# Performance work log

Measured on AMD Instinct MI355X. Metric: run time of the kernel, lower is better.

## Reference

```python
import jax, jax.numpy as jnp
import numpy as np

ALPHA = 0.2  # LeakyReLU negative slope (init arg `alpha`)
N, F_IN, F_OUT = 8192, 512, 256


def setup_inputs() -> dict:
    key = jax.random.key(0)
    k1, k2, k3, k4 = jax.random.split(key, 4)
    x = jax.random.normal(k1, (N, F_IN), dtype=jnp.float32)
    adj = jax.random.randint(k2, (N, N), 0, 2, dtype=jnp.int32)
    W = jax.random.normal(k3, (F_IN, F_OUT), dtype=jnp.float32) * (1.0 / np.sqrt(F_IN))
    a = jax.random.normal(k4, (2 * F_OUT, 1), dtype=jnp.float32) * (1.0 / np.sqrt(F_IN))
    return {"x": x, "adj": adj, "W": W, "a": a}


def reference(x, adj, W, a):
    h = x @ W  # [N, F_OUT]
    f_out = W.shape[1]
    # e[i,j] = LeakyReLU(a1 . h_i + a2 . h_j); computed without the O(N^2*2F) concat
    f1 = h @ a[:f_out, 0]   # [N]
    f2 = h @ a[f_out:, 0]   # [N]
    s = f1[:, None] + f2[None, :]  # [N, N]
    e = jnp.where(s >= 0, s, ALPHA * s)
    # Faithful to the source bug: -9e15 * zeros_like == zeros, so masked entries are 0.0
    att = jnp.where(adj > 0, e, jnp.zeros((), dtype=e.dtype))
    att = jax.nn.softmax(att, axis=1)
    # dropout is identity in eval mode
    h_prime = att @ h  # [N, F_OUT]
    return jax.nn.elu(h_prime)  # concat=True branch
```

## Files before the change

### kernel.cpp

```cpp
#include <hip/hip_runtime.h>
#include <stdint.h>

#define NN 8192
#define FIN 512
#define FOUT 256
#define ALPHA 0.2f
#define KSPLIT 4

typedef float f32x4 __attribute__((ext_vector_type(4)));
typedef short s16x8 __attribute__((ext_vector_type(8)));

__device__ __forceinline__ uint16_t f2bf(float f) {
  union { float f; uint32_t u; } v; v.f = f;
  uint32_t u = v.u + 0x7fffu + ((v.u >> 16) & 1u);
  return (uint16_t)(u >> 16);
}

__global__ __launch_bounds__(256) void k_wa(const float* __restrict__ W,
                                            const float* __restrict__ a,
                                            float* __restrict__ wa1, float* __restrict__ wa2) {
  __shared__ float a1[256], a2[256];
  int tid = threadIdx.x;
  a1[tid] = a[tid];
  a2[tid] = a[tid + 256];
  __syncthreads();
  int m = blockIdx.x * 256 + tid;
  const float* wrow = W + (size_t)m * FOUT;
  float s1 = 0.f, s2 = 0.f;
  for (int k = 0; k < FOUT; k += 4) {
    f32x4 v = *(const f32x4*)(wrow + k);
#pragma unroll
    for (int i = 0; i < 4; i++) {
      s1 += v[i] * a1[k + i];
      s2 += v[i] * a2[k + i];
    }
  }
  wa1[m] = s1; wa2[m] = s2;
}

__global__ __launch_bounds__(256) void k_f1f2(const float* __restrict__ x,
                                              const float* __restrict__ wa1,
                                              const float* __restrict__ wa2,
                                              float* __restrict__ f1, float* __restrict__ f2,
                                              float* __restrict__ e1p, float* __restrict__ e1n,
                                              float* __restrict__ e2p, float* __restrict__ e2n,
                                              uint16_t* __restrict__ xb,
                                              float* __restrict__ l_arr) {
  __shared__ float s1[512], s2[512];
  int tid = threadIdx.x;
  if (tid < 4) l_arr[blockIdx.x * 4 + tid] = 0.f;
  s1[tid] = wa1[tid]; s1[tid + 256] = wa1[tid + 256];
  s2[tid] = wa2[tid]; s2[tid + 256] = wa2[tid + 256];
  __syncthreads();
  int w = tid >> 6, l = tid & 63;
  int row = blockIdx.x * 4 + w;
  const float* xr = x + (size_t)row * FIN + l * 8;
  f32x4 v0 = *(const f32x4*)xr;
  f32x4 v1 = *(const f32x4*)(xr + 4);
  uint4 pk;
  pk.x = (uint32_t)f2bf(v0[0]) | ((uint32_t)f2bf(v0[1]) << 16);
  pk.y = (uint32_t)f2bf(v0[2]) | ((uint32_t)f2bf(v0[3]) << 16);
  pk.z = (uint32_t)f2bf(v1[0]) | ((uint32_t)f2bf(v1[1]) << 16);
  pk.w = (uint32_t)f2bf(v1[2]) | ((uint32_t)f2bf(v1[3]) << 16);
  *(uint4*)(xb + (size_t)row * FIN + l * 8) = pk;
  int kb = l * 8;
  float d1 = 0.f, d2 = 0.f;
#pragma unroll
  for (int i = 0; i < 4; i++) {
    d1 += v0[i] * s1[kb + i] + v1[i] * s1[kb + 4 + i];
    d2 += v0[i] * s2[kb + i] + v1[i] * s2[kb + 4 + i];
  }
#pragma unroll
  for (int off = 32; off; off >>= 1) {
    d1 += __shfl_down(d1, off);
    d2 += __shfl_down(d2, off);
  }
  if (l == 0) {
    f1[row] = d1; f2[row] = d2;
    e1p[row] = __expf(d1);
    e1n[row] = __expf(ALPHA * d1);
    e2p[row] = __expf(d2);
    e2n[row] = __expf(ALPHA * d2);
  }
}

__global__ __launch_bounds__(256) void k_prep_wt(const float* __restrict__ W,
                                                 uint16_t* __restrict__ wt) {
  int idx = blockIdx.x * 256 + threadIdx.x;
  int f  = idx >> 7;
  int k4 = (idx & 127) * 4;
  ushort4 o;
  o.x = f2bf(W[(size_t)(k4 + 0) * FOUT + f]);
  o.y = f2bf(W[(size_t)(k4 + 1) * FOUT + f]);
  o.z = f2bf(W[(size_t)(k4 + 2) * FOUT + f]);
  o.w = f2bf(W[(size_t)(k4 + 3) * FOUT + f]);
  *(ushort4*)(wt + (size_t)f * FIN + k4) = o;
}

__global__ __launch_bounds__(256, 2) void k_gemm_h(const uint16_t* __restrict__ xb,
                                                   const uint16_t* __restrict__ wt,
                                                   uint16_t* __restrict__ h) {
  __shared__ uint16_t Xs[64][40];
  __shared__ uint16_t Ws[128][40];
  int i0 = blockIdx.x * 64;
  int f0 = blockIdx.y * 128;
  int tid = threadIdx.x;
  int w = tid >> 6, l = tid & 63;
  int wr = w >> 1, wc = w & 1;
  int q = l >> 4, r16 = l & 15;
  f32x4 acc[2][4];
#pragma unroll
  for (int a = 0; a < 2; a++)
#pragma unroll
    for (int b = 0; b < 4; b++) acc[a][b] = (f32x4)0.f;

  int srow = tid >> 2, sch = tid & 3;
  for (int k0 = 0; k0 < FIN; k0 += 32) {
    uint4 xv = *(const uint4*)(xb + (size_t)(i0 + srow) * FIN + k0 + sch * 8);
    *(uint4*)(&Xs[srow][sch * 8]) = xv;
#pragma unroll
    for (int r = 0; r < 2; r++) {
      int idx = tid + r * 256;
      int rr = idx >> 2, cc = idx & 3;
      uint4 vw = *(const uint4*)(wt + (size_t)(f0 + rr) * FIN + k0 + cc * 8);
      *(uint4*)(&Ws[rr][cc * 8]) = vw;
    }
    __syncthreads();
    s16x8 A[2], B[4];
#pragma unroll
    for (int a = 0; a < 2; a++) A[a] = *(const s16x8*)(&Xs[wr * 32 + a * 16 + r16][q * 8]);
#pragma unroll
    for (int b = 0; b < 4; b++) B[b] = *(const s16x8*)(&Ws[wc * 64 + b * 16 + r16][q * 8]);
#pragma unroll
    for (int a = 0; a < 2; a++)
#pragma unroll
      for (int b = 0; b < 4; b++)
        acc[a][b] = __builtin_amdgcn_mfma_f32_16x16x32_bf16(A[a], B[b], acc[a][b], 0, 0, 0);
    __syncthreads();
  }
#pragma unroll
  for (int a = 0; a < 2; a++)
#pragma unroll
    for (int b = 0; b < 4; b++)
#pragma unroll
      for (int reg = 0; reg < 4; reg++) {
        int row = i0 + wr * 32 + a * 16 + q * 4 + reg;
        int col = f0 + wc * 64 + b * 16 + r16;
        h[(size_t)row * FOUT + col] = f2bf(acc[a][b][reg]);
      }
}

__global__ __launch_bounds__(256) void k_transpose(const uint16_t* __restrict__ h,
                                                   uint16_t* __restrict__ ht) {
  __shared__ uint16_t T[64][72];
  int i0 = blockIdx.x * 64, f0 = blockIdx.y * 64;
  int tid = threadIdx.x;
#pragma unroll
  for (int p = 0; p < 2; p++) {
    int idx = tid + p * 256;
    int r = idx >> 3, c8 = idx & 7;
    uint4 v = *(const uint4*)(h + (size_t)(i0 + r) * FOUT + f0 + c8 * 8);
    *(uint4*)(&T[r][c8 * 8]) = v;
  }
  __syncthreads();
#pragma unroll
  for (int p = 0; p < 2; p++) {
    int idx = tid + p * 256;
    int fr = idx >> 3, ic8 = idx & 7;
    s16x8 v;
#pragma unroll
    for (int j = 0; j < 8; j++) v[j] = (short)T[ic8 * 8 + j][fr];
    *(s16x8*)(ht + (size_t)(f0 + fr) * NN + i0 + ic8 * 8) = v;
  }
}

__global__ __launch_bounds__(256, 2) void k_att(const int* __restrict__ adj,
                                                const uint16_t* __restrict__ ht,
                                                const float* __restrict__ f1,
                                                const float* __restrict__ f2,
                                                const float* __restrict__ e1p,
                                                const float* __restrict__ e1n,
                                                const float* __restrict__ e2p,
                                                const float* __restrict__ e2n,
                                                float* __restrict__ l_arr,
                                                float* __restrict__ part) {
  __shared__ uint16_t Ps[64][72];
  __shared__ uint16_t Hs[256][72];
  int i0 = blockIdx.x * 64;
  int jbase = blockIdx.y * (NN / KSPLIT);
  int tid = threadIdx.x;
  int w = tid >> 6, l = tid & 63;
  int q = l >> 4, r16 = l & 15;
  int prow = tid >> 2, pch = tid & 3;
  int srow = tid >> 3, sch = tid & 7;
  float negf1 = -f1[i0 + prow];
  float e1pi = e1p[i0 + prow];
  float e1ni = e1n[i0 + prow];
  float lsum = 0.f;
  f32x4 acc[4][4];
#pragma unroll
  for (int a = 0; a < 4; a++)
#pragma unroll
    for (int b = 0; b < 4; b++) acc[a][b] = (f32x4)0.f;

  for (int s = 0; s < NN / KSPLIT; s += 64) {
    int j0 = jbase + s;
    uint4 hv[8];
#pragma unroll
    for (int p = 0; p < 8; p++)
      hv[p] = *(const uint4*)(ht + (size_t)(p * 32 + srow) * NN + j0 + sch * 8);
    const int* ap = adj + (size_t)(i0 + prow) * NN + j0 + pch * 16;
    int4 A0 = *(const int4*)ap;
    int4 A1 = *(const int4*)(ap + 4);
    int4 A2 = *(const int4*)(ap + 8);
    int4 A3 = *(const int4*)(ap + 12);
    const float* fp = f2 + j0 + pch * 16;
    f32x4 F0 = *(const f32x4*)fp;
    f32x4 F1 = *(const f32x4*)(fp + 4);
    f32x4 F2 = *(const f32x4*)(fp + 8);
    f32x4 F3 = *(const f32x4*)(fp + 12);
    const float* gp = e2p + j0 + pch * 16;
    f32x4 P0 = *(const f32x4*)gp;
    f32x4 P1 = *(const f32x4*)(gp + 4);
    f32x4 P2 = *(const f32x4*)(gp + 8);
    f32x4 P3 = *(const f32x4*)(gp + 12);
    const float* gn = e2n + j0 + pch * 16;
    f32x4 Q0 = *(const f32x4*)gn;
    f32x4 Q1 = *(const f32x4*)(gn + 4);
    f32x4 Q2 = *(const f32x4*)(gn + 8);
    f32x4 Q3 = *(const f32x4*)(gn + 12);
    s16x8 pv0, pv1;
#define PC(dst, kk, Ac, Fc, Pc, Nc) { bool c_ = (Fc) >= negf1; \
      float p_ = ((Ac) != 0) ? (c_ ? e1pi : e1ni) * (c_ ? (Pc) : (Nc)) : 1.0f; \
      lsum += p_; dst[kk] = (short)f2bf(p_); }
    PC(pv0, 0, A0.x, F0[0], P0[0], Q0[0]); PC(pv0, 1, A0.y, F0[1], P0[1], Q0[1]);
    PC(pv0, 2, A0.z, F0[2], P0[2], Q0[2]); PC(pv0, 3, A0.w, F0[3], P0[3], Q0[3]);
    PC(pv0, 4, A1.x, F1[0], P1[0], Q1[0]); PC(pv0, 5, A1.y, F1[1], P1[1], Q1[1]);
    PC(pv0, 6, A1.z, F1[2], P1[2], Q1[2]); PC(pv0, 7, A1.w, F1[3], P1[3], Q1[3]);
    PC(pv1, 0, A2.x, F2[0], P2[0], Q2[0]); PC(pv1, 1, A2.y, F2[1], P2[1], Q2[1]);
    PC(pv1, 2, A2.z, F2[2], P2[2], Q2[2]); PC(pv1, 3, A2.w, F2[3], P2[3], Q2[3]);
    PC(pv1, 4, A3.x, F3[0], P3[0], Q3[0]); PC(pv1, 5, A3.y, F3[1], P3[1], Q3[1]);
    PC(pv1, 6, A3.z, F3[2], P3[2], Q3[2]); PC(pv1, 7, A3.w, F3[3], P3[3], Q3[3]);
#undef PC
    *(s16x8*)(&Ps[prow][pch * 16]) = pv0;
    *(s16x8*)(&Ps[prow][pch * 16 + 8]) = pv1;
#pragma unroll
    for (int p = 0; p < 8; p++)
      *(uint4*)(&Hs[p * 32 + srow][sch * 8]) = hv[p];
    __syncthreads();
#pragma unroll
    for (int c = 0; c < 2; c++) {
      s16x8 Af[4], Bf[4];
#pragma unroll
      for (int a = 0; a < 4; a++) Af[a] = *(const s16x8*)(&Ps[a * 16 + r16][c * 32 + q * 8]);
#pragma unroll
      for (int b = 0; b < 4; b++) Bf[b] = *(const s16x8*)(&Hs[w * 64 + b * 16 + r16][c * 32 + q * 8]);
#pragma unroll
      for (int a = 0; a < 4; a++)
#pragma unroll
        for (int b = 0; b < 4; b++)
          acc[a][b] = __builtin_amdgcn_mfma_f32_16x16x32_bf16(Af[a], Bf[b], acc[a][b], 0, 0, 0);
    }
    __syncthreads();
  }

  lsum += __shfl_down(lsum, 2);
  lsum += __shfl_down(lsum, 1);
  if (pch == 0) atomicAdd(&l_arr[i0 + prow], lsum);

  float* pb = part + (size_t)blockIdx.y * ((size_t)NN * FOUT);
#pragma unroll
  for (int a = 0; a < 4; a++)
#pragma unroll
    for (int b = 0; b < 4; b++)
#pragma unroll
      for (int reg = 0; reg < 4; reg++) {
        int row = i0 + a * 16 + q * 4 + reg;
        int col = w * 64 + b * 16 + r16;
        pb[(size_t)row * FOUT + col] = acc[a][b][reg];
      }
}

__global__ __launch_bounds__(256) void k_combine(const float* __restrict__ part,
                                                 const float* __restrict__ l_arr,
                                                 float* __restrict__ out) {
  int idx = (blockIdx.x * 256 + threadIdx.x) * 4;
  float r = 1.0f / l_arr[idx >> 8];
  f32x4 v0 = *(const f32x4*)(part + 0 * (size_t)(NN * FOUT) + idx);
  f32x4 v1 = *(const f32x4*)(part + 1 * (size_t)(NN * FOUT) + idx);
  f32x4 v2 = *(const f32x4*)(part + 2 * (size_t)(NN * FOUT) + idx);
  f32x4 v3 = *(const f32x4*)(part + 3 * (size_t)(NN * FOUT) + idx);
  f32x4 o;
#pragma unroll
  for (int i = 0; i < 4; i++) {
    float v = (v0[i] + v1[i] + v2[i] + v3[i]) * r;
    o[i] = v > 0.f ? v : (__expf(v) - 1.f);
  }
  *(f32x4*)(out + idx) = o;
}

extern "C" void kernel_launch(void* const* d_in, const int* in_sizes, int n_in,
                              void* d_out, int out_size, void* d_ws, size_t ws_size,
                              hipStream_t stream) {
  const float* x   = (const float*)d_in[0];
  const int*   adj = (const int*)d_in[1];
  const float* W   = (const float*)d_in[2];
  const float* a   = (const float*)d_in[3];
  float* out = (float*)d_out;

  char* ws = (char*)d_ws;
  float*    wa1   = (float*)ws;
  float*    wa2   = wa1 + 512;
  float*    f1    = wa2 + 512;
  float*    f2    = f1 + NN;
  float*    l_arr = f2 + NN;
  float*    e1p   = l_arr + NN;
  float*    e1n   = e1p + NN;
  float*    e2p   = e1n + NN;
  float*    e2n   = e2p + NN;
  uint16_t* wt    = (uint16_t*)(e2n + NN);
  uint16_t* xb    = wt + (size_t)FOUT * FIN;
  uint16_t* h     = xb + (size_t)NN * FIN;
  uint16_t* ht    = h + (size_t)NN * FOUT;
  float*    part  = (float*)(ht + (size_t)NN * FOUT);

  k_wa<<<2, 256, 0, stream>>>(W, a, wa1, wa2);
  k_f1f2<<<NN / 4, 256, 0, stream>>>(x, wa1, wa2, f1, f2, e1p, e1n, e2p, e2n, xb, l_arr);
  k_prep_wt<<<128, 256, 0, stream>>>(W, wt);
  k_gemm_h<<<dim3(NN / 64, 2), 256, 0, stream>>>(xb, wt, h);
  k_transpose<<<dim3(NN / 64, FOUT / 64), 256, 0, stream>>>(h, ht);
  k_att<<<dim3(NN / 64, KSPLIT), 256, 0, stream>>>(adj, ht, f1, f2, e1p, e1n, e2p, e2n, l_arr, part);
  k_combine<<<NN * FOUT / 1024, 256, 0, stream>>>(part, l_arr, out);
}
```

Measured before the change: 522.7 us.

## Restructure attention kernel with adjacency prefetch, double-buffered P, direct H fragment loads

The attention kernel now prefetches the next adjacency tile into registers while computing the current one, and double-buffers the probability tile in shared memory. It drops the shared-memory staging of H and reads B fragments straight from global memory. The j-split doubles to 8 and occupancy is raised to 3 blocks per CU, to expose more parallelism and cut synchronisation. The e2 exponentials are packed as two bf16 values in one word to halve those loads, at some precision cost. The H GEMM tile shrinks to 64x64 for more blocks, and the combine kernel reads twice as many partial buffers.

```diff
diff --git a/kernel.cpp b/kernel.cpp
--- a/kernel.cpp
+++ b/kernel.cpp
@@ -5,10 +5,13 @@
 #define FIN 512
 #define FOUT 256
 #define ALPHA 0.2f
-#define KSPLIT 4
+#define KSPLIT 8
+#define JT 64
+#define NT ((NN / KSPLIT) / JT)
 
 typedef float f32x4 __attribute__((ext_vector_type(4)));
 typedef short s16x8 __attribute__((ext_vector_type(8)));
+typedef uint32_t u32x4 __attribute__((ext_vector_type(4)));
 
 __device__ __forceinline__ uint16_t f2bf(float f) {
   union { float f; uint32_t u; } v; v.f = f;
@@ -43,7 +46,7 @@
                                               const float* __restrict__ wa2,
                                               float* __restrict__ f1, float* __restrict__ f2,
                                               float* __restrict__ e1p, float* __restrict__ e1n,
-                                              float* __restrict__ e2p, float* __restrict__ e2n,
+                                              uint32_t* __restrict__ epack,
                                               uint16_t* __restrict__ xb,
                                               float* __restrict__ l_arr) {
   __shared__ float s1[512], s2[512];
@@ -79,8 +82,7 @@
     f1[row] = d1; f2[row] = d2;
     e1p[row] = __expf(d1);
     e1n[row] = __expf(ALPHA * d1);
-    e2p[row] = __expf(d2);
-    e2n[row] = __expf(ALPHA * d2);
+    epack[row] = ((uint32_t)f2bf(__expf(d2)) << 16) | (uint32_t)f2bf(__expf(ALPHA * d2));
   }
 }
 
@@ -101,53 +103,40 @@
                                                    const uint16_t* __restrict__ wt,
                                                    uint16_t* __restrict__ h) {
   __shared__ uint16_t Xs[64][40];
-  __shared__ uint16_t Ws[128][40];
+  __shared__ uint16_t Ws[64][40];
   int i0 = blockIdx.x * 64;
-  int f0 = blockIdx.y * 128;
+  int f0 = blockIdx.y * 64;
   int tid = threadIdx.x;
   int w = tid >> 6, l = tid & 63;
-  int wr = w >> 1, wc = w & 1;
   int q = l >> 4, r16 = l & 15;
-  f32x4 acc[2][4];
-#pragma unroll
-  for (int a = 0; a < 2; a++)
-#pragma unroll
-    for (int b = 0; b < 4; b++) acc[a][b] = (f32x4)0.f;
+  f32x4 acc[4];
+#pragma unroll
+  for (int b = 0; b < 4; b++) acc[b] = (f32x4)0.f;
 
   int srow = tid >> 2, sch = tid & 3;
   for (int k0 = 0; k0 < FIN; k0 += 32) {
     uint4 xv = *(const uint4*)(xb + (size_t)(i0 + srow) * FIN + k0 + sch * 8);
+    uint4 wv = *(const uint4*)(wt + (size_t)(f0 + srow) * FIN + k0 + sch * 8);
     *(uint4*)(&Xs[srow][sch * 8]) = xv;
-#pragma unroll
-    for (int r = 0; r < 2; r++) {
-      int idx = tid + r * 256;
-      int rr = idx >> 2, cc = idx & 3;
-      uint4 vw = *(const uint4*)(wt + (size_t)(f0 + rr) * FIN + k0 + cc * 8);
-      *(uint4*)(&Ws[rr][cc * 8]) = vw;
+    *(uint4*)(&Ws[srow][sch * 8]) = wv;
+    __syncthreads();
+    s16x8 A = *(const s16x8*)(&Xs[w * 16 + r16][q * 8]);
+    s16x8 B[4];
+#pragma unroll
+    for (int b = 0; b < 4; b++) B[b] = *(const s16x8*)(&Ws[b * 16 + r16][q * 8]);
+#pragma unroll
+    for (int b = 0; b < 4; b++)
+      acc[b] = __builtin_amdgcn_mfma_f32_16x16x32_bf16(A, B[b], acc[b], 0, 0, 0);
+    __syncthreads();
+  }
+#pragma unroll
+  for (int b = 0; b < 4; b++)
+#pragma unroll
+    for (int reg = 0; reg < 4; reg++) {
+      int row = i0 + w * 16 + q * 4 + reg;
+      int col = f0 + b * 16 + r16;
+      h[(size_t)row * FOUT + col] = f2bf(acc[b][reg]);
     }
-    __syncthreads();
-    s16x8 A[2], B[4];
-#pragma unroll
-    for (int a = 0; a < 2; a++) A[a] = *(const s16x8*)(&Xs[wr * 32 + a * 16 + r16][q * 8]);
-#pragma unroll
-    for (int b = 0; b < 4; b++) B[b] = *(const s16x8*)(&Ws[wc * 64 + b * 16 + r16][q * 8]);
-#pragma unroll
-    for (int a = 0; a < 2; a++)
-#pragma unroll
-      for (int b = 0; b < 4; b++)
-        acc[a][b] = __builtin_amdgcn_mfma_f32_16x16x32_bf16(A[a], B[b], acc[a][b], 0, 0, 0);
-    __syncthreads();
-  }
-#pragma unroll
-  for (int a = 0; a < 2; a++)
-#pragma unroll
-    for (int b = 0; b < 4; b++)
-#pragma unroll
-      for (int reg = 0; reg < 4; reg++) {
-        int row = i0 + wr * 32 + a * 16 + q * 4 + reg;
-        int col = f0 + wc * 64 + b * 16 + r16;
-        h[(size_t)row * FOUT + col] = f2bf(acc[a][b][reg]);
-      }
 }
 
 __global__ __launch_bounds__(256) void k_transpose(const uint16_t* __restrict__ h,
@@ -174,94 +163,85 @@
   }
 }
 
-__global__ __launch_bounds__(256, 2) void k_att(const int* __restrict__ adj,
+#define ATT_ITER(S, CUR, NXT, PB) { \
+  int j0 = jbase + (S) * JT; \
+  f32x4 F_[4]; \
+  uint4 E_[4]; \
+  const float* fp_ = f2 + j0 + pch * 16; \
+  const uint4* ep_ = (const uint4*)(epack + j0 + pch * 16); \
+  _Pragma("unroll") for (int t = 0; t < 4; ++t) F_[t] = *(const f32x4*)(fp_ + t * 4); \
+  _Pragma("unroll") for (int t = 0; t < 4; ++t) E_[t] = ep_[t]; \
+  s16x8 pv0, pv1; \
+  _Pragma("unroll") for (int t = 0; t < 4; ++t) { \
+    _Pragma("unroll") for (int k2 = 0; k2 < 4; ++k2) { \
+      uint32_t wrd = ((const uint32_t*)&E_[t])[k2]; \
+      float ep2 = __uint_as_float(wrd & 0xffff0000u); \
+      float en2 = __uint_as_float(wrd << 16); \
+      bool c_ = F_[t][k2] >= negf1; \
+      float p_ = (CUR[t][k2] != 0u) ? (c_ ? e1pi * ep2 : e1ni * en2) : 1.0f; \
+      lsum += p_; \
+      uint16_t pb_ = f2bf(p_); \
+      int jj = t * 4 + k2; \
+      if (jj < 8) pv0[jj] = (short)pb_; else pv1[jj - 8] = (short)pb_; \
+    } \
+  } \
+  *(s16x8*)(&Ps[PB][prow][pch * 16]) = pv0; \
+  *(s16x8*)(&Ps[PB][prow][pch * 16 + 8]) = pv1; \
+  if ((S) + 1 < NT) { \
+    const u32x4* ap_ = (const u32x4*)(arow + jbase + ((S) + 1) * JT); \
+    _Pragma("unroll") for (int t = 0; t < 4; ++t) NXT[t] = ap_[t]; \
+  } \
+  __syncthreads(); \
+  for (int c = 0; c < 2; ++c) { \
+    s16x8 Af[4], Bf[4]; \
+    _Pragma("unroll") for (int b = 0; b < 4; ++b) \
+      Bf[b] = *(const s16x8*)(hb + (size_t)(b * 16) * NN + j0 + c * 32); \
+    _Pragma("unroll") for (int a = 0; a < 4; ++a) \
+      Af[a] = *(const s16x8*)(&Ps[PB][a * 16 + r16][c * 32 + q * 8]); \
+    _Pragma("unroll") for (int a = 0; a < 4; ++a) { \
+      _Pragma("unroll") for (int b = 0; b < 4; ++b) \
+        acc[a][b] = __builtin_amdgcn_mfma_f32_16x16x32_bf16(Af[a], Bf[b], acc[a][b], 0, 0, 0); \
+    } \
+  } \
+}
+
+__global__ __launch_bounds__(256, 3) void k_att(const int* __restrict__ adj,
                                                 const uint16_t* __restrict__ ht,
                                                 const float* __restrict__ f1,
                                                 const float* __restrict__ f2,
                                                 const float* __restrict__ e1p,
                                                 const float* __restrict__ e1n,
-                                                const float* __restrict__ e2p,
-                                                const float* __restrict__ e2n,
+                                                const uint32_t* __restrict__ epack,
                                                 float* __restrict__ l_arr,
                                                 float* __restrict__ part) {
-  __shared__ uint16_t Ps[64][72];
-  __shared__ uint16_t Hs[256][72];
+  __shared__ uint16_t Ps[2][64][72];
   int i0 = blockIdx.x * 64;
   int jbase = blockIdx.y * (NN / KSPLIT);
   int tid = threadIdx.x;
   int w = tid >> 6, l = tid & 63;
   int q = l >> 4, r16 = l & 15;
   int prow = tid >> 2, pch = tid & 3;
-  int srow = tid >> 3, sch = tid & 7;
   float negf1 = -f1[i0 + prow];
   float e1pi = e1p[i0 + prow];
   float e1ni = e1n[i0 + prow];
   float lsum = 0.f;
+  const int* arow = adj + (size_t)(i0 + prow) * NN + pch * 16;
+  const uint16_t* hb = ht + (size_t)(w * 64 + r16) * NN + q * 8;
   f32x4 acc[4][4];
 #pragma unroll
   for (int a = 0; a < 4; a++)
 #pragma unroll
     for (int b = 0; b < 4; b++) acc[a][b] = (f32x4)0.f;
 
-  for (int s = 0; s < NN / KSPLIT; s += 64) {
-    int j0 = jbase + s;
-    uint4 hv[8];
-#pragma unroll
-    for (int p = 0; p < 8; p++)
-      hv[p] = *(const uint4*)(ht + (size_t)(p * 32 + srow) * NN + j0 + sch * 8);
-    const int* ap = adj + (size_t)(i0 + prow) * NN + j0 + pch * 16;
-    int4 A0 = *(const int4*)ap;
-    int4 A1 = *(const int4*)(ap + 4);
-    int4 A2 = *(const int4*)(ap + 8);
-    int4 A3 = *(const int4*)(ap + 12);
-    const float* fp = f2 + j0 + pch * 16;
-    f32x4 F0 = *(const f32x4*)fp;
-    f32x4 F1 = *(const f32x4*)(fp + 4);
-    f32x4 F2 = *(const f32x4*)(fp + 8);
-    f32x4 F3 = *(const f32x4*)(fp + 12);
-    const float* gp = e2p + j0 + pch * 16;
-    f32x4 P0 = *(const f32x4*)gp;
-    f32x4 P1 = *(const f32x4*)(gp + 4);
-    f32x4 P2 = *(const f32x4*)(gp + 8);
-    f32x4 P3 = *(const f32x4*)(gp + 12);
-    const float* gn = e2n + j0 + pch * 16;
-    f32x4 Q0 = *(const f32x4*)gn;
-    f32x4 Q1 = *(const f32x4*)(gn + 4);
-    f32x4 Q2 = *(const f32x4*)(gn + 8);
-    f32x4 Q3 = *(const f32x4*)(gn + 12);
-    s16x8 pv0, pv1;
-#define PC(dst, kk, Ac, Fc, Pc, Nc) { bool c_ = (Fc) >= negf1; \
-      float p_ = ((Ac) != 0) ? (c_ ? e1pi : e1ni) * (c_ ? (Pc) : (Nc)) : 1.0f; \
-      lsum += p_; dst[kk] = (short)f2bf(p_); }
-    PC(pv0, 0, A0.x, F0[0], P0[0], Q0[0]); PC(pv0, 1, A0.y, F0[1], P0[1], Q0[1]);
-    PC(pv0, 2, A0.z, F0[2], P0[2], Q0[2]); PC(pv0, 3, A0.w, F0[3], P0[3], Q0[3]);
-    PC(pv0, 4, A1.x, F1[0], P1[0], Q1[0]); PC(pv0, 5, A1.y, F1[1], P1[1], Q1[1]);
-    PC(pv0, 6, A1.z, F1[2], P1[2], Q1[2]); PC(pv0, 7, A1.w, F1[3], P1[3], Q1[3]);
-    PC(pv1, 0, A2.x, F2[0], P2[0], Q2[0]); PC(pv1, 1, A2.y, F2[1], P2[1], Q2[1]);
-    PC(pv1, 2, A2.z, F2[2], P2[2], Q2[2]); PC(pv1, 3, A2.w, F2[3], P2[3], Q2[3]);
-    PC(pv1, 4, A3.x, F3[0], P3[0], Q3[0]); PC(pv1, 5, A3.y, F3[1], P3[1], Q3[1]);
-    PC(pv1, 6, A3.z, F3[2], P3[2], Q3[2]); PC(pv1, 7, A3.w, F3[3], P3[3], Q3[3]);
-#undef PC
-    *(s16x8*)(&Ps[prow][pch * 16]) = pv0;
-    *(s16x8*)(&Ps[prow][pch * 16 + 8]) = pv1;
-#pragma unroll
-    for (int p = 0; p < 8; p++)
-      *(uint4*)(&Hs[p * 32 + srow][sch * 8]) = hv[p];
-    __syncthreads();
-#pragma unroll
-    for (int c = 0; c < 2; c++) {
-      s16x8 Af[4], Bf[4];
-#pragma unroll
-      for (int a = 0; a < 4; a++) Af[a] = *(const s16x8*)(&Ps[a * 16 + r16][c * 32 + q * 8]);
-#pragma unroll
-      for (int b = 0; b < 4; b++) Bf[b] = *(const s16x8*)(&Hs[w * 64 + b * 16 + r16][c * 32 + q * 8]);
-#pragma unroll
-      for (int a = 0; a < 4; a++)
-#pragma unroll
-        for (int b = 0; b < 4; b++)
-          acc[a][b] = __builtin_amdgcn_mfma_f32_16x16x32_bf16(Af[a], Bf[b], acc[a][b], 0, 0, 0);
-    }
-    __syncthreads();
+  u32x4 adv0[4], adv1[4];
+  {
+    const u32x4* ap_ = (const u32x4*)(arow + jbase);
+#pragma unroll
+    for (int t = 0; t < 4; ++t) adv0[t] = ap_[t];
+  }
+  for (int s = 0; s < NT; s += 2) {
+    ATT_ITER(s,     adv0, adv1, 0)
+    ATT_ITER(s + 1, adv1, adv0, 1)
   }
 
   lsum += __shfl_down(lsum, 2);
@@ -286,14 +266,14 @@
                                                  float* __restrict__ out) {
   int idx = (blockIdx.x * 256 + threadIdx.x) * 4;
   float r = 1.0f / l_arr[idx >> 8];
-  f32x4 v0 = *(const f32x4*)(part + 0 * (size_t)(NN * FOUT) + idx);
-  f32x4 v1 = *(const f32x4*)(part + 1 * (size_t)(NN * FOUT) + idx);
-  f32x4 v2 = *(const f32x4*)(part + 2 * (size_t)(NN * FOUT) + idx);
-  f32x4 v3 = *(const f32x4*)(part + 3 * (size_t)(NN * FOUT) + idx);
+  f32x4 sum = (f32x4)0.f;
+#pragma unroll
+  for (int p = 0; p < KSPLIT; p++)
+    sum += *(const f32x4*)(part + (size_t)p * (NN * FOUT) + idx);
   f32x4 o;
 #pragma unroll
   for (int i = 0; i < 4; i++) {
-    float v = (v0[i] + v1[i] + v2[i] + v3[i]) * r;
+    float v = sum[i] * r;
     o[i] = v > 0.f ? v : (__expf(v) - 1.f);
   }
   *(f32x4*)(out + idx) = o;
@@ -316,19 +296,18 @@
   float*    l_arr = f2 + NN;
   float*    e1p   = l_arr + NN;
   float*    e1n   = e1p + NN;
-  float*    e2p   = e1n + NN;
-  float*    e2n   = e2p + NN;
-  uint16_t* wt    = (uint16_t*)(e2n + NN);
+  uint32_t* epack = (uint32_t*)(e1n + NN);
+  uint16_t* wt    = (uint16_t*)(epack + NN);
   uint16_t* xb    = wt + (size_t)FOUT * FIN;
   uint16_t* h     = xb + (size_t)NN * FIN;
   uint16_t* ht    = h + (size_t)NN * FOUT;
   float*    part  = (float*)(ht + (size_t)NN * FOUT);
 
   k_wa<<<2, 256, 0, stream>>>(W, a, wa1, wa2);
-  k_f1f2<<<NN / 4, 256, 0, stream>>>(x, wa1, wa2, f1, f2, e1p, e1n, e2p, e2n, xb, l_arr);
+  k_f1f2<<<NN / 4, 256, 0, stream>>>(x, wa1, wa2, f1, f2, e1p, e1n, epack, xb, l_arr);
   k_prep_wt<<<128, 256, 0, stream>>>(W, wt);
-  k_gemm_h<<<dim3(NN / 64, 2), 256, 0, stream>>>(xb, wt, h);
+  k_gemm_h<<<dim3(NN / 64, FOUT / 64), 256, 0, stream>>>(xb, wt, h);
   k_transpose<<<dim3(NN / 64, FOUT / 64), 256, 0, stream>>>(h, ht);
-  k_att<<<dim3(NN / 64, KSPLIT), 256, 0, stream>>>(adj, ht, f1, f2, e1p, e1n, e2p, e2n, l_arr, part);
+  k_att<<<dim3(NN / 64, KSPLIT), 256, 0, stream>>>(adj, ht, f1, f2, e1p, e1n, epack, l_arr, part);
   k_combine<<<NN * FOUT / 1024, 256, 0, stream>>>(part, l_arr, out);
 }
```

Result: slower. 616.3 us (+17.9%).
